# Performance work log

Hardware: AMD Instinct MI355X
Metric: run time of the kernel (lower is better)

The kernel has to match this reference:

```python
import jax, jax.numpy as jnp
import numpy as np

RMS_EPS = 1e-6


def setup_inputs() -> dict:
    key = jax.random.key(0)
    ks = jax.random.split(key, 6)
    B, S, D, F, E = 4, 2048, 1024, 4096, 8
    scale = 0.02
    return {
        "hidden_states": jax.random.normal(ks[0], (B, S, D), dtype=jnp.float32),
        "norm_weight": jnp.ones((D,), dtype=jnp.float32),
        "gate_w": jax.random.normal(ks[1], (E, D), dtype=jnp.float32) * scale,
        "w1": jax.random.normal(ks[2], (E, D, F), dtype=jnp.float32) * scale,
        "w3": jax.random.normal(ks[3], (E, D, F), dtype=jnp.float32) * scale,
        "w2": jax.random.normal(ks[4], (E, F, D), dtype=jnp.float32) * scale,
        "top_k": 2,
    }


def reference(hidden_states, norm_weight, gate_w, w1, w3, w2, top_k):
    B, S, D = hidden_states.shape
    E = gate_w.shape[0]
    # norm_fn: RMSNorm (pre-MoE norm in Mixtral block)
    x = hidden_states * jax.lax.rsqrt(jnp.mean(jnp.square(hidden_states), axis=-1, keepdims=True) + RMS_EPS)
    x = (x * norm_weight).reshape(-1, D)  # [T, D], T = B*S
    # router
    router_logits = jnp.einsum('td,ed->te', x, gate_w)  # [T, E]
    routing = jax.nn.softmax(router_logits.astype(jnp.float32), axis=-1)
    top_w, top_idx = jax.lax.top_k(routing, top_k)  # [T, k]
    top_w = top_w / jnp.sum(top_w, axis=-1, keepdims=True)
    top_w = top_w.astype(x.dtype)
    # dense-masked expert combine: tokens not routed to expert e get weight 0,
    # mathematically identical to the gather/scatter loop in the original.
    out = jnp.zeros_like(x)
    for e in range(E):  # fixed small loop over experts
        w_e = jnp.sum(jnp.where(top_idx == e, top_w, 0.0), axis=-1)  # [T]
        h = jax.nn.silu(x @ w1[e]) * (x @ w3[e])  # [T, F] SwiGLU expert
        out = out + w_e[:, None] * (h @ w2[e])
    return out.reshape(B, S, D), router_logits
```

## Files before the change

kernel.cpp:

```cpp
#include <hip/hip_runtime.h>
#include <hip/hip_bf16.h>

#define T_TOK 8192
#define D_DIM 1024
#define F_DIM 4096
#define E_NUM 8

typedef short s16x8 __attribute__((ext_vector_type(8)));
typedef float f32x4 __attribute__((ext_vector_type(4)));
typedef unsigned short u16x8 __attribute__((ext_vector_type(8)));

__device__ __forceinline__ unsigned short f2bf(float f) {
  union { float f; unsigned int u; } v; v.f = f;
  unsigned int u = v.u;
  return (unsigned short)((u + 0x7FFFu + ((u >> 16) & 1u)) >> 16);
}

__device__ __forceinline__ void async16(const void* g, void* l) {
  __builtin_amdgcn_global_load_lds((const __attribute__((address_space(1))) void*)g,
                                   (__attribute__((address_space(3))) void*)l, 16, 0, 0);
}

__global__ __launch_bounds__(256) void prepass_kernel(
    const float* __restrict__ hs, const float* __restrict__ nw,
    const float* __restrict__ gw, const float* __restrict__ w1,
    const float* __restrict__ w3, const float* __restrict__ w2,
    unsigned short* __restrict__ xb, unsigned short* __restrict__ w13t,
    unsigned short* __restrict__ w2t, float* __restrict__ logits_out,
    int* __restrict__ cnt, int* __restrict__ ilist, float* __restrict__ wlist) {
  __shared__ unsigned short tileS[64][72];
  __shared__ float red[4];
  __shared__ float pl[4][8];
  int bx = blockIdx.x;
  int tid = threadIdx.x;
  if (bx < 24576) {
    int tensor = bx >> 13;
    int e = (bx >> 10) & 7;
    int tl = bx & 1023;
    const float* src; int C, tr, tc;
    if (tensor == 0) {
      src = w1 + (size_t)e * D_DIM * F_DIM; C = F_DIM; tr = tl >> 6; tc = tl & 63;
    } else if (tensor == 1) {
      src = w3 + (size_t)e * D_DIM * F_DIM; C = F_DIM; tr = tl >> 6; tc = tl & 63;
    } else {
      src = w2 + (size_t)e * F_DIM * D_DIM; C = D_DIM; tr = tl >> 4; tc = tl & 15;
    }
    int r0 = tr * 64, c0 = tc * 64;
    int rr = tid >> 4, ccb = (tid & 15) * 4;
#pragma unroll
    for (int i = 0; i < 4; ++i) {
      int r = rr + i * 16;
      float4 v = *(const float4*)(src + (size_t)(r0 + r) * C + c0 + ccb);
      tileS[ccb + 0][r] = f2bf(v.x);
      tileS[ccb + 1][r] = f2bf(v.y);
      tileS[ccb + 2][r] = f2bf(v.z);
      tileS[ccb + 3][r] = f2bf(v.w);
    }
    __syncthreads();
    int row = tid >> 2, col = (tid & 3) * 16;
    unsigned short* dp;
    if (tensor < 2) {
      int f = c0 + row;
      int prow = ((f >> 5) * 64) + (f & 31) + (tensor == 1 ? 32 : 0);
      dp = w13t + ((size_t)e * 8192 + prow) * D_DIM + r0 + col;
    } else {
      dp = w2t + ((size_t)e * D_DIM + c0 + row) * F_DIM + r0 + col;
    }
    u16x8 v0, v1;
#pragma unroll
    for (int j = 0; j < 8; ++j) { v0[j] = tileS[row][col + j]; v1[j] = tileS[row][col + 8 + j]; }
    *(u16x8*)dp = v0;
    *(u16x8*)(dp + 8) = v1;
  } else {
    int t = bx - 24576;
    int lane = tid & 63, wid = tid >> 6;
    float4 v = ((const float4*)(hs + (size_t)t * D_DIM))[tid];
    float ss = v.x * v.x + v.y * v.y + v.z * v.z + v.w * v.w;
#pragma unroll
    for (int o = 32; o > 0; o >>= 1) ss += __shfl_xor(ss, o);
    if (lane == 0) red[wid] = ss;
    __syncthreads();
    float ms = (red[0] + red[1] + red[2] + red[3]) * (1.0f / 1024.0f);
    float rs = rsqrtf(ms + 1e-6f);
    float4 wv = ((const float4*)nw)[tid];
    float x0 = v.x * rs * wv.x, x1 = v.y * rs * wv.y;
    float x2 = v.z * rs * wv.z, x3 = v.w * rs * wv.w;
    ((ushort4*)(xb + (size_t)t * D_DIM))[tid] =
        make_ushort4(f2bf(x0), f2bf(x1), f2bf(x2), f2bf(x3));
    float p[8];
#pragma unroll
    for (int e = 0; e < 8; ++e) {
      float4 g = ((const float4*)(gw + (size_t)e * D_DIM))[tid];
      p[e] = x0 * g.x + x1 * g.y + x2 * g.z + x3 * g.w;
    }
#pragma unroll
    for (int e = 0; e < 8; ++e) {
#pragma unroll
      for (int o = 32; o > 0; o >>= 1) p[e] += __shfl_xor(p[e], o);
    }
    if (lane == 0) {
#pragma unroll
      for (int e = 0; e < 8; ++e) pl[wid][e] = p[e];
    }
    __syncthreads();
    if (tid == 0) {
      float l[8];
#pragma unroll
      for (int e = 0; e < 8; ++e) {
        l[e] = pl[0][e] + pl[1][e] + pl[2][e] + pl[3][e];
        logits_out[(size_t)t * 8 + e] = l[e];
      }
      int i0 = 0; float b0 = l[0];
#pragma unroll
      for (int e = 1; e < 8; ++e) if (l[e] > b0) { b0 = l[e]; i0 = e; }
      int i1 = (i0 == 0) ? 1 : 0; float b1 = l[i1];
#pragma unroll
      for (int e = 0; e < 8; ++e) if (e != i0 && l[e] > b1) { b1 = l[e]; i1 = e; }
      float wa = 1.0f / (1.0f + __expf(b1 - b0));
      float wb = 1.0f / (1.0f + __expf(b0 - b1));
      int p0 = atomicAdd(&cnt[i0], 1);
      ilist[i0 * T_TOK + p0] = t * 2;     wlist[i0 * T_TOK + p0] = wa;
      int p1 = atomicAdd(&cnt[i1], 1);
      ilist[i1 * T_TOK + p1] = t * 2 + 1; wlist[i1 * T_TOK + p1] = wb;
    }
  }
}

__global__ __launch_bounds__(512, 2) void gemm1_kernel(
    const unsigned short* __restrict__ xb, const unsigned short* __restrict__ w13t,
    unsigned short* __restrict__ H, const int* __restrict__ cnt,
    const int* __restrict__ ilist) {
  int flat = blockIdx.x;
  int e = flat & 7;
  int work = flat >> 3;
  int rt = work & 31;
  int ft = work >> 5;
  int ne = cnt[e];
  int r0 = rt * 256;
  if (r0 >= ne) return;
  __shared__ __align__(16) unsigned short As[3 * 8192];
  __shared__ __align__(16) unsigned short Bs[3 * 8192];
  __shared__ int toks[256];
  int tid = threadIdx.x, lane = tid & 63, w = tid >> 6;
  if (tid < 256) toks[tid] = ilist[e * T_TOK + min(r0 + tid, ne - 1)];
  __syncthreads();
  const unsigned short* bpanel = w13t + ((size_t)e * 8192 + ft * 256) * D_DIM;
  int sr0 = tid >> 2, sr1 = sr0 + 128;
  int ch0 = (((tid & 3) ^ ((sr0 >> 1) & 3)) * 8);
  int ch1 = (((tid & 3) ^ ((sr1 >> 1) & 3)) * 8);
  const unsigned short* ap0 = xb + (size_t)(toks[sr0] >> 1) * D_DIM + ch0;
  const unsigned short* ap1 = xb + (size_t)(toks[sr1] >> 1) * D_DIM + ch1;
  const unsigned short* bp0 = bpanel + (size_t)sr0 * D_DIM + ch0;
  const unsigned short* bp1 = bpanel + (size_t)sr1 * D_DIM + ch1;
  int d0 = (sr0 * 32) + (tid & 3) * 8;
  int d1 = d0 + 4096;
  int wr = w >> 2, wc = w & 3;
  int lr = lane & 15, lc = lane >> 4;
  int aoff[8], boff[4];
#pragma unroll
  for (int m = 0; m < 8; ++m) {
    int row = wr * 128 + m * 16 + lr;
    aoff[m] = row * 32 + ((lc ^ ((row >> 1) & 3)) * 8);
  }
#pragma unroll
  for (int n = 0; n < 4; ++n) {
    int row = wc * 64 + n * 16 + lr;
    boff[n] = row * 32 + ((lc ^ ((row >> 1) & 3)) * 8);
  }
  f32x4 acc[8][4] = {};
  async16(ap0, &As[d0]); async16(ap1, &As[d1]);
  async16(bp0, &Bs[d0]); async16(bp1, &Bs[d1]);
  async16(ap0 + 32, &As[8192 + d0]); async16(ap1 + 32, &As[8192 + d1]);
  async16(bp0 + 32, &Bs[8192 + d0]); async16(bp1 + 32, &Bs[8192 + d1]);

#define G1_STEP(T_, BUF_, VMC_, DOST_)                                          \
  {                                                                             \
    asm volatile("s_waitcnt vmcnt(" VMC_ ")" ::: "memory");                     \
    __builtin_amdgcn_s_barrier();                                               \
    const unsigned short* Ab = &As[(BUF_) * 8192];                              \
    const unsigned short* Bb = &Bs[(BUF_) * 8192];                              \
    s16x8 a[8], b[4];                                                           \
    if (DOST_) {                                   \
      int nk = ((T_) + 2) * 32;                                                 \
      async16(ap0 + nk, &As[(((BUF_) + 2) % 3) * 8192 + d0]);                   \
      async16(ap1 + nk, &As[(((BUF_) + 2) % 3) * 8192 + d1]);                   \
    }                                                                           \
    _Pragma("unroll") for (int m = 0; m < 4; ++m)                               \
        a[m] = *(const s16x8*)(Ab + aoff[m]);                                   \
    _Pragma("unroll") for (int n = 0; n < 4; ++n)                               \
        b[n] = *(const s16x8*)(Bb + boff[n]);                                   \
    __builtin_amdgcn_s_setprio(1);                                              \
    _Pragma("unroll") for (int m = 0; m < 4; ++m)                               \
        _Pragma("unroll") for (int n = 0; n < 4; ++n)                           \
            acc[m][n] = __builtin_amdgcn_mfma_f32_16x16x32_bf16(                \
                a[m], b[n], acc[m][n], 0, 0, 0);                                \
    __builtin_amdgcn_s_setprio(0);                                              \
    if (DOST_) {                                   \
      int nk = ((T_) + 2) * 32;                                                 \
      async16(bp0 + nk, &Bs[(((BUF_) + 2) % 3) * 8192 + d0]);                   \
      async16(bp1 + nk, &Bs[(((BUF_) + 2) % 3) * 8192 + d1]);                   \
    }                                                                           \
    _Pragma("unroll") for (int m = 4; m < 8; ++m)                               \
        a[m] = *(const s16x8*)(Ab + aoff[m]);                                   \
    __builtin_amdgcn_s_setprio(1);                                              \
    _Pragma("unroll") for (int m = 4; m < 8; ++m)                               \
        _Pragma("unroll") for (int n = 0; n < 4; ++n)                           \
            acc[m][n] = __builtin_amdgcn_mfma_f32_16x16x32_bf16(                \
                a[m], b[n], acc[m][n], 0, 0, 0);                                \
    __builtin_amdgcn_s_setprio(0);                                              \
  }

  for (int tb = 0; tb < 30; tb += 3) {
    G1_STEP(tb, 0, "4", 1)
    G1_STEP(tb + 1, 1, "4", 1)
    G1_STEP(tb + 2, 2, "4", 1)
  }
  G1_STEP(30, 0, "4", 0)
  G1_STEP(31, 1, "0", 0)
#undef G1_STEP

  int g4 = lane >> 4, cl = lane & 15;
  int fbase = (4 * ft + wc) * 32;
#pragma unroll
  for (int m = 0; m < 8; ++m) {
#pragma unroll
    for (int j = 0; j < 4; ++j) {
      int rloc = wr * 128 + m * 16 + g4 * 4 + j;
      if (r0 + rloc < ne) {
        unsigned short* hp = H + (size_t)toks[rloc] * F_DIM + fbase + cl;
#pragma unroll
        for (int n = 0; n < 2; ++n) {
          float c1 = acc[m][n][j], c3 = acc[m][n + 2][j];
          float h = c1 / (1.0f + __expf(-c1)) * c3;
          hp[n * 16] = f2bf(h);
        }
      }
    }
  }
}

__global__ __launch_bounds__(512, 2) void gemm2_kernel(
    const unsigned short* __restrict__ H, const unsigned short* __restrict__ w2t,
    const int* __restrict__ cnt, const int* __restrict__ ilist,
    const float* __restrict__ wlist, float* __restrict__ out) {
  int flat = blockIdx.x;
  int e = flat & 7;
  int work = flat >> 3;
  int rt = work & 31;
  int nt = work >> 5;
  int ne = cnt[e];
  int r0 = rt * 256;
  if (r0 >= ne) return;
  __shared__ __align__(16) unsigned short As[3 * 8192];
  __shared__ __align__(16) unsigned short Bs[3 * 8192];
  __shared__ int toks[256];
  __shared__ float wts[256];
  int tid = threadIdx.x, lane = tid & 63, w = tid >> 6;
  if (tid < 256) {
    int idx = e * T_TOK + min(r0 + tid, ne - 1);
    toks[tid] = ilist[idx];
    wts[tid] = wlist[idx];
  }
  __syncthreads();
  const unsigned short* bpanel = w2t + ((size_t)e * D_DIM + nt * 256) * F_DIM;
  int sr0 = tid >> 2, sr1 = sr0 + 128;
  int ch0 = (((tid & 3) ^ ((sr0 >> 1) & 3)) * 8);
  int ch1 = (((tid & 3) ^ ((sr1 >> 1) & 3)) * 8);
  const unsigned short* ap0 = H + (size_t)toks[sr0] * F_DIM + ch0;
  const unsigned short* ap1 = H + (size_t)toks[sr1] * F_DIM + ch1;
  const unsigned short* bp0 = bpanel + (size_t)sr0 * F_DIM + ch0;
  const unsigned short* bp1 = bpanel + (size_t)sr1 * F_DIM + ch1;
  int d0 = (sr0 * 32) + (tid & 3) * 8;
  int d1 = d0 + 4096;
  int wr = w >> 2, wc = w & 3;
  int lr = lane & 15, lc = lane >> 4;
  int aoff[8], boff[4];
#pragma unroll
  for (int m = 0; m < 8; ++m) {
    int row = wr * 128 + m * 16 + lr;
    aoff[m] = row * 32 + ((lc ^ ((row >> 1) & 3)) * 8);
  }
#pragma unroll
  for (int n = 0; n < 4; ++n) {
    int row = wc * 64 + n * 16 + lr;
    boff[n] = row * 32 + ((lc ^ ((row >> 1) & 3)) * 8);
  }
  f32x4 acc[8][4] = {};
  async16(ap0, &As[d0]); async16(ap1, &As[d1]);
  async16(bp0, &Bs[d0]); async16(bp1, &Bs[d1]);
  async16(ap0 + 32, &As[8192 + d0]); async16(ap1 + 32, &As[8192 + d1]);
  async16(bp0 + 32, &Bs[8192 + d0]); async16(bp1 + 32, &Bs[8192 + d1]);

#define G2_STEP(T_, BUF_, VMC_, DOST_)                                          \
  {                                                                             \
    asm volatile("s_waitcnt vmcnt(" VMC_ ")" ::: "memory");                     \
    __builtin_amdgcn_s_barrier();                                               \
    const unsigned short* Ab = &As[(BUF_) * 8192];                              \
    const unsigned short* Bb = &Bs[(BUF_) * 8192];                              \
    s16x8 a[8], b[4];                                                           \
    if (DOST_) {                                                                \
      int nk = ((T_) + 2) * 32;                                                 \
      async16(ap0 + nk, &As[(((BUF_) + 2) % 3) * 8192 + d0]);                   \
      async16(ap1 + nk, &As[(((BUF_) + 2) % 3) * 8192 + d1]);                   \
    }                                                                           \
    _Pragma("unroll") for (int m = 0; m < 4; ++m)                               \
        a[m] = *(const s16x8*)(Ab + aoff[m]);                                   \
    _Pragma("unroll") for (int n = 0; n < 4; ++n)                               \
        b[n] = *(const s16x8*)(Bb + boff[n]);                                   \
    __builtin_amdgcn_s_setprio(1);                                              \
    _Pragma("unroll") for (int m = 0; m < 4; ++m)                               \
        _Pragma("unroll") for (int n = 0; n < 4; ++n)                           \
            acc[m][n] = __builtin_amdgcn_mfma_f32_16x16x32_bf16(                \
                a[m], b[n], acc[m][n], 0, 0, 0);                                \
    __builtin_amdgcn_s_setprio(0);                                              \
    if (DOST_) {                                                                \
      int nk = ((T_) + 2) * 32;                                                 \
      async16(bp0 + nk, &Bs[(((BUF_) + 2) % 3) * 8192 + d0]);                   \
      async16(bp1 + nk, &Bs[(((BUF_) + 2) % 3) * 8192 + d1]);                   \
    }                                                                           \
    _Pragma("unroll") for (int m = 4; m < 8; ++m)                               \
        a[m] = *(const s16x8*)(Ab + aoff[m]);                                   \
    __builtin_amdgcn_s_setprio(1);                                              \
    _Pragma("unroll") for (int m = 4; m < 8; ++m)                               \
        _Pragma("unroll") for (int n = 0; n < 4; ++n)                           \
            acc[m][n] = __builtin_amdgcn_mfma_f32_16x16x32_bf16(                \
                a[m], b[n], acc[m][n], 0, 0, 0);                                \
    __builtin_amdgcn_s_setprio(0);                                              \
  }

  for (int tb = 0; tb < 126; tb += 3) {
    G2_STEP(tb, 0, "4", 1)
    G2_STEP(tb + 1, 1, "4", 1)
    G2_STEP(tb + 2, 2, "4", 1)
  }
  G2_STEP(126, 0, "4", 0)
  G2_STEP(127, 1, "0", 0)
#undef G2_STEP

  int g4 = lane >> 4, cl = lane & 15;
#pragma unroll
  for (int m = 0; m < 8; ++m) {
#pragma unroll
    for (int j = 0; j < 4; ++j) {
      int rloc = wr * 128 + m * 16 + g4 * 4 + j;
      if (r0 + rloc < ne) {
        int tok = toks[rloc] >> 1;
        float ww = wts[rloc];
        float* op = out + (size_t)tok * D_DIM + nt * 256 + wc * 64 + cl;
#pragma unroll
        for (int n = 0; n < 4; ++n)
          unsafeAtomicAdd(op + n * 16, ww * acc[m][n][j]);
      }
    }
  }
}

extern "C" void kernel_launch(void* const* d_in, const int* in_sizes, int n_in,
                              void* d_out, int out_size, void* d_ws, size_t ws_size,
                              hipStream_t stream) {
  const float* hs = (const float*)d_in[0];
  const float* nw = (const float*)d_in[1];
  const float* gw = (const float*)d_in[2];
  const float* w1 = (const float*)d_in[3];
  const float* w3 = (const float*)d_in[4];
  const float* w2 = (const float*)d_in[5];
  float* out = (float*)d_out;
  float* logits_out = out + (size_t)T_TOK * D_DIM;

  char* ws = (char*)d_ws;
  unsigned short* xb   = (unsigned short*)(ws);
  unsigned short* w13t = (unsigned short*)(ws + 16777216ull);
  unsigned short* w2t  = (unsigned short*)(ws + 150994944ull);
  unsigned short* H    = (unsigned short*)(ws + 218103808ull);
  int*   ilist = (int*)(ws + 352321536ull);
  float* wlist = (float*)(ws + 352583680ull);
  int*   cnt   = (int*)(ws + 352845824ull);

  hipMemsetAsync(out, 0, (size_t)T_TOK * D_DIM * sizeof(float), stream);
  hipMemsetAsync(cnt, 0, E_NUM * sizeof(int), stream);
  prepass_kernel<<<24576 + T_TOK, 256, 0, stream>>>(
      hs, nw, gw, w1, w3, w2, xb, w13t, w2t, logits_out, cnt, ilist, wlist);
  gemm1_kernel<<<E_NUM * 32 * 32, 512, 0, stream>>>(xb, w13t, H, cnt, ilist);
  gemm2_kernel<<<E_NUM * 32 * 4, 512, 0, stream>>>(H, w2t, cnt, ilist, wlist, out);
}
```

Before: 904.7 us.

## Deepen GEMM LDS pipeline to four stages and vectorize gemm1 epilogue stores

Both expert GEMM kernels move from a 3-stage to a 4-stage LDS ring, prefetching three K-tiles ahead with adjusted vmcnt waits to hide more global-load latency. The gemm1 epilogue now stages SwiGLU outputs through per-wave LDS regions and writes 16-byte nontemporal vector stores instead of scattered 2-byte stores. The cost is more LDS per block (128KB) and extra LDS traffic in the epilogue.

```diff
diff --git a/kernel.cpp b/kernel.cpp
--- a/kernel.cpp
+++ b/kernel.cpp
@@ -138,8 +138,8 @@
   int ne = cnt[e];
   int r0 = rt * 256;
   if (r0 >= ne) return;
-  __shared__ __align__(16) unsigned short As[3 * 8192];
-  __shared__ __align__(16) unsigned short Bs[3 * 8192];
+  __shared__ __align__(16) unsigned short As[4 * 8192];
+  __shared__ __align__(16) unsigned short Bs[4 * 8192];
   __shared__ int toks[256];
   int tid = threadIdx.x, lane = tid & 63, w = tid >> 6;
   if (tid < 256) toks[tid] = ilist[e * T_TOK + min(r0 + tid, ne - 1)];
@@ -168,10 +168,12 @@
     boff[n] = row * 32 + ((lc ^ ((row >> 1) & 3)) * 8);
   }
   f32x4 acc[8][4] = {};
-  async16(ap0, &As[d0]); async16(ap1, &As[d1]);
-  async16(bp0, &Bs[d0]); async16(bp1, &Bs[d1]);
-  async16(ap0 + 32, &As[8192 + d0]); async16(ap1 + 32, &As[8192 + d1]);
-  async16(bp0 + 32, &Bs[8192 + d0]); async16(bp1 + 32, &Bs[8192 + d1]);
+  async16(ap0, &As[d0]);               async16(ap1, &As[d1]);
+  async16(bp0, &Bs[d0]);               async16(bp1, &Bs[d1]);
+  async16(ap0 + 32, &As[8192 + d0]);   async16(ap1 + 32, &As[8192 + d1]);
+  async16(bp0 + 32, &Bs[8192 + d0]);   async16(bp1 + 32, &Bs[8192 + d1]);
+  async16(ap0 + 64, &As[16384 + d0]);  async16(ap1 + 64, &As[16384 + d1]);
+  async16(bp0 + 64, &Bs[16384 + d0]);  async16(bp1 + 64, &Bs[16384 + d1]);
 
 #define G1_STEP(T_, BUF_, VMC_, DOST_)                                          \
   {                                                                             \
@@ -180,10 +182,10 @@
     const unsigned short* Ab = &As[(BUF_) * 8192];                              \
     const unsigned short* Bb = &Bs[(BUF_) * 8192];                              \
     s16x8 a[8], b[4];                                                           \
-    if (DOST_) {                                   \
-      int nk = ((T_) + 2) * 32;                                                 \
-      async16(ap0 + nk, &As[(((BUF_) + 2) % 3) * 8192 + d0]);                   \
-      async16(ap1 + nk, &As[(((BUF_) + 2) % 3) * 8192 + d1]);                   \
+    if (DOST_) {            \
+      int nk = ((T_) + 3) * 32;                                                 \
+      async16(ap0 + nk, &As[(((BUF_) + 3) & 3) * 8192 + d0]);                   \
+      async16(ap1 + nk, &As[(((BUF_) + 3) & 3) * 8192 + d1]);                   \
     }                                                                           \
     _Pragma("unroll") for (int m = 0; m < 4; ++m)                               \
         a[m] = *(const s16x8*)(Ab + aoff[m]);                                   \
@@ -195,10 +197,10 @@
             acc[m][n] = __builtin_amdgcn_mfma_f32_16x16x32_bf16(                \
                 a[m], b[n], acc[m][n], 0, 0, 0);                                \
     __builtin_amdgcn_s_setprio(0);                                              \
-    if (DOST_) {                                   \
-      int nk = ((T_) + 2) * 32;                                                 \
-      async16(bp0 + nk, &Bs[(((BUF_) + 2) % 3) * 8192 + d0]);                   \
-      async16(bp1 + nk, &Bs[(((BUF_) + 2) % 3) * 8192 + d1]);                   \
+    if (DOST_) {                                       \
+      int nk = ((T_) + 3) * 32;                                                 \
+      async16(bp0 + nk, &Bs[(((BUF_) + 3) & 3) * 8192 + d0]);                   \
+      async16(bp1 + nk, &Bs[(((BUF_) + 3) & 3) * 8192 + d1]);                   \
     }                                                                           \
     _Pragma("unroll") for (int m = 4; m < 8; ++m)                               \
         a[m] = *(const s16x8*)(Ab + aoff[m]);                                   \
@@ -210,32 +212,49 @@
     __builtin_amdgcn_s_setprio(0);                                              \
   }
 
-  for (int tb = 0; tb < 30; tb += 3) {
-    G1_STEP(tb, 0, "4", 1)
-    G1_STEP(tb + 1, 1, "4", 1)
-    G1_STEP(tb + 2, 2, "4", 1)
-  }
-  G1_STEP(30, 0, "4", 0)
-  G1_STEP(31, 1, "0", 0)
+  for (int tb = 0; tb < 28; tb += 4) {
+    G1_STEP(tb + 0, 0, "8", 1)
+    G1_STEP(tb + 1, 1, "8", 1)
+    G1_STEP(tb + 2, 2, "8", 1)
+    G1_STEP(tb + 3, 3, "8", 1)
+  }
+  G1_STEP(28, 0, "8", 1)
+  G1_STEP(29, 1, "8", 0)
+  G1_STEP(30, 2, "4", 0)
+  G1_STEP(31, 3, "0", 0)
 #undef G1_STEP
 
   int g4 = lane >> 4, cl = lane & 15;
   int fbase = (4 * ft + wc) * 32;
-#pragma unroll
-  for (int m = 0; m < 8; ++m) {
-#pragma unroll
-    for (int j = 0; j < 4; ++j) {
-      int rloc = wr * 128 + m * 16 + g4 * 4 + j;
-      if (r0 + rloc < ne) {
-        unsigned short* hp = H + (size_t)toks[rloc] * F_DIM + fbase + cl;
+  unsigned short* Hs = (unsigned short*)As;
+  int c8 = lane & 3;
+#pragma unroll
+  for (int p = 0; p < 2; ++p) {
+#pragma unroll
+    for (int mm = 0; mm < 4; ++mm) {
+      int m = p * 4 + mm;
+#pragma unroll
+      for (int j = 0; j < 4; ++j) {
+        int rl = mm * 16 + g4 * 4 + j;
 #pragma unroll
         for (int n = 0; n < 2; ++n) {
           float c1 = acc[m][n][j], c3 = acc[m][n + 2][j];
-          float h = c1 / (1.0f + __expf(-c1)) * c3;
-          hp[n * 16] = f2bf(h);
+          Hs[w * 2048 + rl * 32 + n * 16 + cl] = f2bf(c1 / (1.0f + __expf(-c1)) * c3);
         }
       }
     }
+    asm volatile("s_waitcnt lgkmcnt(0)" ::: "memory");
+#pragma unroll
+    for (int i = 0; i < 4; ++i) {
+      int rl = (i * 64 + lane) >> 2;
+      int rloc = wr * 128 + p * 64 + rl;
+      if (r0 + rloc < ne) {
+        u16x8 v = *(const u16x8*)&Hs[w * 2048 + rl * 32 + c8 * 8];
+        __builtin_nontemporal_store(
+            v, (u16x8*)(H + (size_t)toks[rloc] * F_DIM + fbase + c8 * 8));
+      }
+    }
+    asm volatile("s_waitcnt lgkmcnt(0)" ::: "memory");
   }
 }
 
@@ -251,8 +270,8 @@
   int ne = cnt[e];
   int r0 = rt * 256;
   if (r0 >= ne) return;
-  __shared__ __align__(16) unsigned short As[3 * 8192];
-  __shared__ __align__(16) unsigned short Bs[3 * 8192];
+  __shared__ __align__(16) unsigned short As[4 * 8192];
+  __shared__ __align__(16) unsigned short Bs[4 * 8192];
   __shared__ int toks[256];
   __shared__ float wts[256];
   int tid = threadIdx.x, lane = tid & 63, w = tid >> 6;
@@ -286,10 +305,12 @@
     boff[n] = row * 32 + ((lc ^ ((row >> 1) & 3)) * 8);
   }
   f32x4 acc[8][4] = {};
-  async16(ap0, &As[d0]); async16(ap1, &As[d1]);
-  async16(bp0, &Bs[d0]); async16(bp1, &Bs[d1]);
-  async16(ap0 + 32, &As[8192 + d0]); async16(ap1 + 32, &As[8192 + d1]);
-  async16(bp0 + 32, &Bs[8192 + d0]); async16(bp1 + 32, &Bs[8192 + d1]);
+  async16(ap0, &As[d0]);               async16(ap1, &As[d1]);
+  async16(bp0, &Bs[d0]);               async16(bp1, &Bs[d1]);
+  async16(ap0 + 32, &As[8192 + d0]);   async16(ap1 + 32, &As[8192 + d1]);
+  async16(bp0 + 32, &Bs[8192 + d0]);   async16(bp1 + 32, &Bs[8192 + d1]);
+  async16(ap0 + 64, &As[16384 + d0]);  async16(ap1 + 64, &As[16384 + d1]);
+  async16(bp0 + 64, &Bs[16384 + d0]);  async16(bp1 + 64, &Bs[16384 + d1]);
 
 #define G2_STEP(T_, BUF_, VMC_, DOST_)                                          \
   {                                                                             \
@@ -299,9 +320,9 @@
     const unsigned short* Bb = &Bs[(BUF_) * 8192];                              \
     s16x8 a[8], b[4];                                                           \
     if (DOST_) {                                                                \
-      int nk = ((T_) + 2) * 32;                                                 \
-      async16(ap0 + nk, &As[(((BUF_) + 2) % 3) * 8192 + d0]);                   \
-      async16(ap1 + nk, &As[(((BUF_) + 2) % 3) * 8192 + d1]);                   \
+      int nk = ((T_) + 3) * 32;                                                 \
+      async16(ap0 + nk, &As[(((BUF_) + 3) & 3) * 8192 + d0]);                   \
+      async16(ap1 + nk, &As[(((BUF_) + 3) & 3) * 8192 + d1]);                   \
     }                                                                           \
     _Pragma("unroll") for (int m = 0; m < 4; ++m)                               \
         a[m] = *(const s16x8*)(Ab + aoff[m]);                                   \
@@ -314,9 +335,9 @@
                 a[m], b[n], acc[m][n], 0, 0, 0);                                \
     __builtin_amdgcn_s_setprio(0);                                              \
     if (DOST_) {                                                                \
-      int nk = ((T_) + 2) * 32;                                                 \
-      async16(bp0 + nk, &Bs[(((BUF_) + 2) % 3) * 8192 + d0]);                   \
-      async16(bp1 + nk, &Bs[(((BUF_) + 2) % 3) * 8192 + d1]);                   \
+      int nk = ((T_) + 3) * 32;                                                 \
+      async16(bp0 + nk, &Bs[(((BUF_) + 3) & 3) * 8192 + d0]);                   \
+      async16(bp1 + nk, &Bs[(((BUF_) + 3) & 3) * 8192 + d1]);                   \
     }                                                                           \
     _Pragma("unroll") for (int m = 4; m < 8; ++m)                               \
         a[m] = *(const s16x8*)(Ab + aoff[m]);                                   \
@@ -328,13 +349,16 @@
     __builtin_amdgcn_s_setprio(0);                                              \
   }
 
-  for (int tb = 0; tb < 126; tb += 3) {
-    G2_STEP(tb, 0, "4", 1)
-    G2_STEP(tb + 1, 1, "4", 1)
-    G2_STEP(tb + 2, 2, "4", 1)
-  }
-  G2_STEP(126, 0, "4", 0)
-  G2_STEP(127, 1, "0", 0)
+  for (int tb = 0; tb < 124; tb += 4) {
+    G2_STEP(tb + 0, 0, "8", 1)
+    G2_STEP(tb + 1, 1, "8", 1)
+    G2_STEP(tb + 2, 2, "8", 1)
+    G2_STEP(tb + 3, 3, "8", 1)
+  }
+  G2_STEP(124, 0, "8", 1)
+  G2_STEP(125, 1, "8", 0)
+  G2_STEP(126, 2, "4", 0)
+  G2_STEP(127, 3, "0", 0)
 #undef G2_STEP
 
   int g4 = lane >> 4, cl = lane & 15;
```

New measurement: 910.6 us. No clear change (+0.6%).
